# Kernel tuning notes

Measured on AMD Instinct MI355X. Metric: run time of the kernel, lower is better.

The kernel has to match this reference:

```python
import jax, jax.numpy as jnp
import numpy as np

LN_EPS = 1e-5  # torch LayerNorm default
MODES = 4


def setup_inputs() -> dict:
    key = jax.random.key(0)
    ks = jax.random.split(key, 5)
    B, S, H = 4, 4096, 1024
    nh, dk = 16, H // 16
    scale = 1.0 / (H * H)
    # frequency mode selection: random shuffle of range(S//2), take 4, sorted (seeded for determinism)
    rng = np.random.default_rng(0)
    index = jnp.asarray(np.sort(rng.permutation(S // 2)[:MODES]).astype(np.int32))
    return {
        "x": jax.random.normal(ks[0], (B, S, H), dtype=jnp.float32),
        "Wq": jax.random.normal(ks[1], (H, H), dtype=jnp.float32) * np.sqrt(2.0 / (H + dk)),
        "bq": jnp.zeros((H,), dtype=jnp.float32),
        "wr": scale * jax.random.uniform(ks[2], (nh, dk, dk, MODES), dtype=jnp.float32),
        "wi": scale * jax.random.uniform(ks[3], (nh, dk, dk, MODES), dtype=jnp.float32),
        "gamma": jnp.ones((H,), dtype=jnp.float32),
        "beta": jnp.zeros((H,), dtype=jnp.float32),
        "index": index,
    }


def reference(x, Wq, bq, wr, wi, gamma, beta, index):
    B, S, H = x.shape
    nh, dk = wr.shape[0], wr.shape[1]
    # q projection and head split: (B,S,H) -> (B,S,nh,dk) -> (B,nh,dk,S)
    q = (x @ Wq.T + bq).reshape(B, S, nh, dk).transpose(0, 2, 3, 1)
    x_ft = jnp.fft.rfft(q, axis=-1)                 # (B,nh,dk,S//2+1) complex
    xm = x_ft[..., index]                           # gather selected modes: (B,nh,dk,M)
    w = wr + 1j * wi                                # (nh,dk,dk,M) complex
    ym = jnp.einsum('bhim,hiom->bhom', xm, w)       # per-mode complex matmul
    # faithful: results written at slots 0..M-1 of out_ft (loop writes out_ft[...,wi])
    out_ft = jnp.zeros((B, nh, dk, S // 2 + 1), dtype=ym.dtype).at[..., :ym.shape[-1]].set(ym)
    x_if = jnp.fft.irfft(out_ft, n=S, axis=-1)      # (B,nh,dk,S) real
    # faithful permute(0,3,2,1).view: flattens as dk-major over heads
    out = x_if.transpose(0, 3, 2, 1).reshape(B, S, H)
    # dropout is identity in eval mode
    y = out + x
    mu = jnp.mean(y, axis=-1, keepdims=True)
    var = jnp.var(y, axis=-1, keepdims=True)
    return (y - mu) * jax.lax.rsqrt(var + LN_EPS) * gamma + beta
```

## Files before the change

kernel.cpp:

```cpp
#include <hip/hip_runtime.h>
#include <math.h>

#define BB 4
#define SS 4096
#define HH 1024
#define NH 16
#define DK 64
#define NMODES 4
#define NSB 128
#define SCHUNK (SS/NSB)
#define PPLANE ((size_t)BB * NSB * HH)
#define TWO_PI 6.28318530717958647692f

__global__ __launch_bounds__(256) void kA_dft(const float* __restrict__ x,
                                              const int* __restrict__ index,
                                              float* __restrict__ P) {
    __shared__ float tab[SCHUNK * 8];
    int t  = threadIdx.x;
    int sb = blockIdx.x & (NSB - 1);
    int b  = blockIdx.x >> 7;

    if (t < SCHUNK * NMODES) {
        int sl = t >> 2, m = t & 3;
        int k  = index[m];
        int sv = sb * SCHUNK + sl;
        int r  = (k * sv) & (SS - 1);
        float ang = (float)r * (TWO_PI / (float)SS);
        float sn, cs;
        sincosf(ang, &sn, &cs);
        tab[sl * 8 + m * 2]     = cs;
        tab[sl * 8 + m * 2 + 1] = sn;
    }
    __syncthreads();

    int c0 = t * 4;
    float acc[4][8];
    #pragma unroll
    for (int e = 0; e < 4; ++e)
        #pragma unroll
        for (int q = 0; q < 8; ++q) acc[e][q] = 0.f;

    const float* xp = x + ((size_t)(b * SS + sb * SCHUNK)) * HH + c0;
    #pragma unroll 4
    for (int r = 0; r < SCHUNK; ++r) {
        float4 xv = *(const float4*)(xp + (size_t)r * HH);
        float4 t0 = *(const float4*)&tab[r * 8];
        float4 t1 = *(const float4*)&tab[r * 8 + 4];
        float xe;
        #pragma unroll
        for (int e = 0; e < 4; ++e) {
            xe = (e == 0) ? xv.x : (e == 1) ? xv.y : (e == 2) ? xv.z : xv.w;
            acc[e][0] += xe * t0.x;  acc[e][1] -= xe * t0.y;
            acc[e][2] += xe * t0.z;  acc[e][3] -= xe * t0.w;
            acc[e][4] += xe * t1.x;  acc[e][5] -= xe * t1.y;
            acc[e][6] += xe * t1.z;  acc[e][7] -= xe * t1.w;
        }
    }
    size_t base = (size_t)(b * NSB + sb) * HH + c0;
    #pragma unroll
    for (int q = 0; q < 8; ++q) {
        *(float4*)&P[q * PPLANE + base] =
            make_float4(acc[0][q], acc[1][q], acc[2][q], acc[3][q]);
    }
}

__global__ __launch_bounds__(256) void kA2_reduce(const float* __restrict__ P,
                                                  float* __restrict__ G) {
    int g = blockIdx.x * 256 + threadIdx.x;
    int j = g & (HH - 1);
    int q = (g >> 10) & 7;
    int b = g >> 13;
    const float* pp = P + q * PPLANE + (size_t)b * NSB * HH + j;
    float s = 0.f;
    #pragma unroll 16
    for (int sb = 0; sb < NSB; ++sb)
        s += pp[(size_t)sb * HH];
    G[g] = s;
}

__global__ __launch_bounds__(256) void kB_proj(const float* __restrict__ Wq,
                                               const float* __restrict__ bq,
                                               const int* __restrict__ index,
                                               const float* __restrict__ G,
                                               float* __restrict__ XM) {
    __shared__ float Gs[8 * HH];
    int t  = threadIdx.x;
    int cb = blockIdx.x & 63;
    int b  = blockIdx.x >> 6;
    {
        const float4* gsrc = (const float4*)(G + (size_t)b * 8 * HH);
        float4* gdst = (float4*)Gs;
        for (int u = t; u < 2 * HH; u += 256) gdst[u] = gsrc[u];
    }
    __syncthreads();

    int cl = t >> 4, jq = t & 15;
    int c = cb * 16 + cl;
    float acc[8] = {0.f,0.f,0.f,0.f,0.f,0.f,0.f,0.f};
    for (int j0 = jq * 4; j0 < HH; j0 += 64) {
        float4 wv = *(const float4*)&Wq[(size_t)c * HH + j0];
        #pragma unroll
        for (int q = 0; q < 8; ++q) {
            float4 gv = *(const float4*)&Gs[q * HH + j0];
            acc[q] += wv.x * gv.x + wv.y * gv.y + wv.z * gv.z + wv.w * gv.w;
        }
    }
    #pragma unroll
    for (int q = 0; q < 8; ++q) {
        acc[q] += __shfl_xor(acc[q], 1);
        acc[q] += __shfl_xor(acc[q], 2);
        acc[q] += __shfl_xor(acc[q], 4);
        acc[q] += __shfl_xor(acc[q], 8);
    }
    if (jq == 0) {
        float bias = bq[c];
        #pragma unroll
        for (int m = 0; m < NMODES; ++m)
            if (index[m] == 0) acc[2 * m] += bias * (float)SS;
        float* o = XM + ((size_t)(b * HH + c)) * 8;
        *(float4*)o       = make_float4(acc[0], acc[1], acc[2], acc[3]);
        *(float4*)(o + 4) = make_float4(acc[4], acc[5], acc[6], acc[7]);
    }
}

#define KC_IQ 8
#define KC_II (DK / KC_IQ)
__global__ __launch_bounds__(512) void kC_modes(const float* __restrict__ wr,
                                                const float* __restrict__ wi,
                                                const float* __restrict__ XM,
                                                float* __restrict__ CF) {
    __shared__ float xs[DK * 8];
    __shared__ float red[KC_IQ][DK][9];
    int t = threadIdx.x;
    int o = t & 63, iq = t >> 6;
    int h = blockIdx.x & 15;
    int b = blockIdx.x >> 4;
    for (int u = t; u < DK * 8; u += 512)
        xs[u] = XM[((size_t)(b * HH + h * DK)) * 8 + u];
    __syncthreads();

    float re[4] = {0.f,0.f,0.f,0.f}, im[4] = {0.f,0.f,0.f,0.f};
    #pragma unroll
    for (int ii = 0; ii < KC_II; ++ii) {
        int i = iq * KC_II + ii;
        float4 wrv = *(const float4*)&wr[(((size_t)(h * DK + i)) * DK + o) * 4];
        float4 wiv = *(const float4*)&wi[(((size_t)(h * DK + i)) * DK + o) * 4];
        float xr, xi;
        xr = xs[i * 8 + 0]; xi = xs[i * 8 + 1];
        re[0] += xr * wrv.x - xi * wiv.x;  im[0] += xr * wiv.x + xi * wrv.x;
        xr = xs[i * 8 + 2]; xi = xs[i * 8 + 3];
        re[1] += xr * wrv.y - xi * wiv.y;  im[1] += xr * wiv.y + xi * wrv.y;
        xr = xs[i * 8 + 4]; xi = xs[i * 8 + 5];
        re[2] += xr * wrv.z - xi * wiv.z;  im[2] += xr * wiv.z + xi * wrv.z;
        xr = xs[i * 8 + 6]; xi = xs[i * 8 + 7];
        re[3] += xr * wrv.w - xi * wiv.w;  im[3] += xr * wiv.w + xi * wrv.w;
    }
    #pragma unroll
    for (int m = 0; m < 4; ++m) {
        red[iq][o][2 * m]     = re[m];
        red[iq][o][2 * m + 1] = im[m];
    }
    __syncthreads();
    if (iq == 0) {
        float rr[8];
        #pragma unroll
        for (int q = 0; q < 8; ++q) {
            float s = 0.f;
            #pragma unroll
            for (int g = 0; g < KC_IQ; ++g) s += red[g][o][q];
            rr[q] = s;
        }
        int co = o * NH + h;
        const float inv = 1.0f / (float)SS;
        float* cp = CF + ((size_t)(b * HH + co)) * 8;
        cp[0] =  rr[0] * inv;
        cp[1] =  2.0f * rr[2] * inv;
        cp[2] = -2.0f * rr[3] * inv;
        cp[3] =  2.0f * rr[4] * inv;
        cp[4] = -2.0f * rr[5] * inv;
        cp[5] =  2.0f * rr[6] * inv;
        cp[6] = -2.0f * rr[7] * inv;
        cp[7] =  0.0f;
    }
}

#define KD_ROWS 16
#define KD_RB 8
__global__ __launch_bounds__(256) void kD_out(const float* __restrict__ x,
                                              const float* __restrict__ CF,
                                              const float* __restrict__ gamma,
                                              const float* __restrict__ beta,
                                              float* __restrict__ out) {
    __shared__ float trig[KD_ROWS][2];
    __shared__ float red[4][KD_RB][2];
    int t  = threadIdx.x;
    int b  = blockIdx.x >> 8;
    int s0 = (blockIdx.x & 255) * KD_ROWS;
    int c0 = t * 4;

    if (t < KD_ROWS) {
        float ang = (float)(s0 + t) * (TWO_PI / (float)SS);
        float sn, cs;
        sincosf(ang, &sn, &cs);
        trig[t][0] = cs;
        trig[t][1] = sn;
    }

    const float* cp = CF + (size_t)b * HH * 8 + (size_t)c0 * 8;
    float4 cfa[8];
    #pragma unroll
    for (int e = 0; e < 4; ++e) {
        cfa[2 * e]     = *(const float4*)(cp + e * 8);
        cfa[2 * e + 1] = *(const float4*)(cp + e * 8 + 4);
    }
    float4 g4 = *(const float4*)&gamma[c0];
    float4 b4 = *(const float4*)&beta[c0];
    int w = t >> 6, lane = t & 63;
    __syncthreads();

    for (int batch = 0; batch < KD_ROWS / KD_RB; ++batch) {
        float4 yv[KD_RB];
        #pragma unroll
        for (int r = 0; r < KD_RB; ++r) {
            int s = s0 + batch * KD_RB + r;
            yv[r] = *(const float4*)&x[((size_t)(b * SS + s)) * HH + c0];
        }
        float sm[KD_RB], sq[KD_RB];
        #pragma unroll
        for (int r = 0; r < KD_RB; ++r) {
            int ri = batch * KD_RB + r;
            float c1 = trig[ri][0], s1 = trig[ri][1];
            float c2 = c1 * c1 - s1 * s1, s2 = 2.f * s1 * c1;
            float c3 = c2 * c1 - s2 * s1, s3 = s2 * c1 + c2 * s1;
            float ye[4];
            #pragma unroll
            for (int e = 0; e < 4; ++e) {
                float xe = (e == 0) ? yv[r].x : (e == 1) ? yv[r].y
                         : (e == 2) ? yv[r].z : yv[r].w;
                float4 A = cfa[2 * e], Bv = cfa[2 * e + 1];
                ye[e] = xe + A.x + A.y * c1 + A.z * s1 + A.w * c2
                           + Bv.x * s2 + Bv.y * c3 + Bv.z * s3;
            }
            yv[r] = make_float4(ye[0], ye[1], ye[2], ye[3]);
            sm[r] = ye[0] + ye[1] + ye[2] + ye[3];
            sq[r] = ye[0]*ye[0] + ye[1]*ye[1] + ye[2]*ye[2] + ye[3]*ye[3];
        }
        #pragma unroll
        for (int off = 1; off < 64; off <<= 1) {
            #pragma unroll
            for (int r = 0; r < KD_RB; ++r) {
                sm[r] += __shfl_xor(sm[r], off);
                sq[r] += __shfl_xor(sq[r], off);
            }
        }
        if (lane == 0) {
            #pragma unroll
            for (int r = 0; r < KD_RB; ++r) {
                red[w][r][0] = sm[r];
                red[w][r][1] = sq[r];
            }
        }
        __syncthreads();
        #pragma unroll
        for (int r = 0; r < KD_RB; ++r) {
            int s = s0 + batch * KD_RB + r;
            float tot  = red[0][r][0] + red[1][r][0] + red[2][r][0] + red[3][r][0];
            float totq = red[0][r][1] + red[1][r][1] + red[2][r][1] + red[3][r][1];
            float mean = tot * (1.0f / (float)HH);
            float var  = totq * (1.0f / (float)HH) - mean * mean;
            float rs = rsqrtf(var + 1e-5f);
            float4 o4;
            o4.x = (yv[r].x - mean) * rs * g4.x + b4.x;
            o4.y = (yv[r].y - mean) * rs * g4.y + b4.y;
            o4.z = (yv[r].z - mean) * rs * g4.z + b4.z;
            o4.w = (yv[r].w - mean) * rs * g4.w + b4.w;
            *(float4*)&out[((size_t)(b * SS + s)) * HH + c0] = o4;
        }
        __syncthreads();
    }
}

extern "C" void kernel_launch(void* const* d_in, const int* in_sizes, int n_in,
                              void* d_out, int out_size, void* d_ws, size_t ws_size,
                              hipStream_t stream) {
    const float* x     = (const float*)d_in[0];
    const float* Wq    = (const float*)d_in[1];
    const float* bq    = (const float*)d_in[2];
    const float* wr    = (const float*)d_in[3];
    const float* wi    = (const float*)d_in[4];
    const float* gamma = (const float*)d_in[5];
    const float* beta  = (const float*)d_in[6];
    const int*   index = (const int*)d_in[7];
    float* out = (float*)d_out;
    float* ws  = (float*)d_ws;

    const size_t nP     = PPLANE * 8;
    const size_t nSmall = (size_t)BB * HH * 8;

    float *P, *G, *XM, *CF;
    if (ws_size >= (nP + 3 * nSmall) * sizeof(float)) {
        P  = ws;
        G  = P + nP;
        XM = G + nSmall;
        CF = XM + nSmall;
    } else {
        P  = out;
        G  = ws;
        XM = G + nSmall;
        CF = XM + nSmall;
    }

    hipLaunchKernelGGL(kA_dft,     dim3(BB * NSB), dim3(256), 0, stream, x, index, P);
    hipLaunchKernelGGL(kA2_reduce, dim3(BB * HH * 8 / 256), dim3(256), 0, stream, P, G);
    hipLaunchKernelGGL(kB_proj,    dim3(BB * 64), dim3(256), 0, stream, Wq, bq, index, G, XM);
    hipLaunchKernelGGL(kC_modes,   dim3(BB * NH), dim3(512), 0, stream, wr, wi, XM, CF);
    hipLaunchKernelGGL(kD_out,     dim3(BB * (SS / KD_ROWS)), dim3(256), 0, stream, x, CF, gamma, beta, out);
}
```

Before: 61.73 us.

## Fuse reduce, projection and mode kernels into one cooperative kernel with grid syncs

Merges the partial-sum reduction, the Wq projection and the per-mode complex matmul into a single cooperative kernel of 256 blocks, separated by grid-wide syncs. This replaces three launches and removes the inter-kernel gaps. The reduction now splits each sum across two threads, and the mode stage runs with 256 threads per block instead of 512. The DFT loop unroll also goes from 4 to 8. The cost is that grid.sync barriers add their own latency, and the mode stage keeps only 64 of the 256 blocks busy.

```diff
diff --git a/kernel.cpp b/kernel.cpp
--- a/kernel.cpp
+++ b/kernel.cpp
@@ -1,5 +1,8 @@
 #include <hip/hip_runtime.h>
+#include <hip/hip_cooperative_groups.h>
 #include <math.h>
+
+namespace cg = cooperative_groups;
 
 #define BB 4
 #define SS 4096
@@ -41,7 +44,7 @@
         for (int q = 0; q < 8; ++q) acc[e][q] = 0.f;
 
     const float* xp = x + ((size_t)(b * SS + sb * SCHUNK)) * HH + c0;
-    #pragma unroll 4
+    #pragma unroll 8
     for (int r = 0; r < SCHUNK; ++r) {
         float4 xv = *(const float4*)(xp + (size_t)r * HH);
         float4 t0 = *(const float4*)&tab[r * 8];
@@ -64,123 +67,130 @@
     }
 }
 
-__global__ __launch_bounds__(256) void kA2_reduce(const float* __restrict__ P,
-                                                  float* __restrict__ G) {
-    int g = blockIdx.x * 256 + threadIdx.x;
-    int j = g & (HH - 1);
-    int q = (g >> 10) & 7;
-    int b = g >> 13;
-    const float* pp = P + q * PPLANE + (size_t)b * NSB * HH + j;
-    float s = 0.f;
-    #pragma unroll 16
-    for (int sb = 0; sb < NSB; ++sb)
-        s += pp[(size_t)sb * HH];
-    G[g] = s;
-}
-
-__global__ __launch_bounds__(256) void kB_proj(const float* __restrict__ Wq,
-                                               const float* __restrict__ bq,
-                                               const int* __restrict__ index,
-                                               const float* __restrict__ G,
-                                               float* __restrict__ XM) {
-    __shared__ float Gs[8 * HH];
-    int t  = threadIdx.x;
-    int cb = blockIdx.x & 63;
-    int b  = blockIdx.x >> 6;
+__global__ __launch_bounds__(256) void kMid(const float* __restrict__ P,
+                                            const float* __restrict__ Wq,
+                                            const float* __restrict__ bq,
+                                            const int* __restrict__ index,
+                                            const float* __restrict__ wr,
+                                            const float* __restrict__ wi,
+                                            float* __restrict__ G,
+                                            float* __restrict__ XM,
+                                            float* __restrict__ CF) {
+    cg::grid_group grid = cg::this_grid();
+    __shared__ float lds[10240];
+    int t = threadIdx.x, bid = blockIdx.x;
+
     {
+        int i = bid * 256 + t;
+        int g = i >> 1;
+        int half = i & 1;
+        int j = g & (HH - 1);
+        int q = (g >> 10) & 7;
+        int b = g >> 13;
+        const float* pp = P + q * PPLANE + (size_t)b * NSB * HH
+                        + (size_t)(half * (NSB / 2)) * HH + j;
+        float s = 0.f;
+        #pragma unroll 16
+        for (int sb = 0; sb < NSB / 2; ++sb)
+            s += pp[(size_t)sb * HH];
+        float other = __shfl_xor(s, 1);
+        if (half == 0) G[g] = s + other;
+    }
+    __threadfence();
+    grid.sync();
+
+    {
+        int cb = bid & 63;
+        int b  = bid >> 6;
         const float4* gsrc = (const float4*)(G + (size_t)b * 8 * HH);
-        float4* gdst = (float4*)Gs;
+        float4* gdst = (float4*)lds;
         for (int u = t; u < 2 * HH; u += 256) gdst[u] = gsrc[u];
-    }
-    __syncthreads();
-
-    int cl = t >> 4, jq = t & 15;
-    int c = cb * 16 + cl;
-    float acc[8] = {0.f,0.f,0.f,0.f,0.f,0.f,0.f,0.f};
-    for (int j0 = jq * 4; j0 < HH; j0 += 64) {
-        float4 wv = *(const float4*)&Wq[(size_t)c * HH + j0];
+        __syncthreads();
+
+        int cl = t >> 4, jq = t & 15;
+        int c = cb * 16 + cl;
+        float acc[8] = {0.f,0.f,0.f,0.f,0.f,0.f,0.f,0.f};
+        for (int j0 = jq * 4; j0 < HH; j0 += 64) {
+            float4 wv = *(const float4*)&Wq[(size_t)c * HH + j0];
+            #pragma unroll
+            for (int q = 0; q < 8; ++q) {
+                float4 gv = *(const float4*)&lds[q * HH + j0];
+                acc[q] += wv.x * gv.x + wv.y * gv.y + wv.z * gv.z + wv.w * gv.w;
+            }
+        }
         #pragma unroll
         for (int q = 0; q < 8; ++q) {
-            float4 gv = *(const float4*)&Gs[q * HH + j0];
-            acc[q] += wv.x * gv.x + wv.y * gv.y + wv.z * gv.z + wv.w * gv.w;
-        }
-    }
-    #pragma unroll
-    for (int q = 0; q < 8; ++q) {
-        acc[q] += __shfl_xor(acc[q], 1);
-        acc[q] += __shfl_xor(acc[q], 2);
-        acc[q] += __shfl_xor(acc[q], 4);
-        acc[q] += __shfl_xor(acc[q], 8);
-    }
-    if (jq == 0) {
-        float bias = bq[c];
-        #pragma unroll
-        for (int m = 0; m < NMODES; ++m)
-            if (index[m] == 0) acc[2 * m] += bias * (float)SS;
-        float* o = XM + ((size_t)(b * HH + c)) * 8;
-        *(float4*)o       = make_float4(acc[0], acc[1], acc[2], acc[3]);
-        *(float4*)(o + 4) = make_float4(acc[4], acc[5], acc[6], acc[7]);
-    }
-}
-
-#define KC_IQ 8
-#define KC_II (DK / KC_IQ)
-__global__ __launch_bounds__(512) void kC_modes(const float* __restrict__ wr,
-                                                const float* __restrict__ wi,
-                                                const float* __restrict__ XM,
-                                                float* __restrict__ CF) {
-    __shared__ float xs[DK * 8];
-    __shared__ float red[KC_IQ][DK][9];
-    int t = threadIdx.x;
-    int o = t & 63, iq = t >> 6;
-    int h = blockIdx.x & 15;
-    int b = blockIdx.x >> 4;
-    for (int u = t; u < DK * 8; u += 512)
-        xs[u] = XM[((size_t)(b * HH + h * DK)) * 8 + u];
-    __syncthreads();
-
-    float re[4] = {0.f,0.f,0.f,0.f}, im[4] = {0.f,0.f,0.f,0.f};
-    #pragma unroll
-    for (int ii = 0; ii < KC_II; ++ii) {
-        int i = iq * KC_II + ii;
-        float4 wrv = *(const float4*)&wr[(((size_t)(h * DK + i)) * DK + o) * 4];
-        float4 wiv = *(const float4*)&wi[(((size_t)(h * DK + i)) * DK + o) * 4];
-        float xr, xi;
-        xr = xs[i * 8 + 0]; xi = xs[i * 8 + 1];
-        re[0] += xr * wrv.x - xi * wiv.x;  im[0] += xr * wiv.x + xi * wrv.x;
-        xr = xs[i * 8 + 2]; xi = xs[i * 8 + 3];
-        re[1] += xr * wrv.y - xi * wiv.y;  im[1] += xr * wiv.y + xi * wrv.y;
-        xr = xs[i * 8 + 4]; xi = xs[i * 8 + 5];
-        re[2] += xr * wrv.z - xi * wiv.z;  im[2] += xr * wiv.z + xi * wrv.z;
-        xr = xs[i * 8 + 6]; xi = xs[i * 8 + 7];
-        re[3] += xr * wrv.w - xi * wiv.w;  im[3] += xr * wiv.w + xi * wrv.w;
-    }
-    #pragma unroll
-    for (int m = 0; m < 4; ++m) {
-        red[iq][o][2 * m]     = re[m];
-        red[iq][o][2 * m + 1] = im[m];
-    }
-    __syncthreads();
-    if (iq == 0) {
-        float rr[8];
-        #pragma unroll
-        for (int q = 0; q < 8; ++q) {
-            float s = 0.f;
-            #pragma unroll
-            for (int g = 0; g < KC_IQ; ++g) s += red[g][o][q];
-            rr[q] = s;
-        }
-        int co = o * NH + h;
-        const float inv = 1.0f / (float)SS;
-        float* cp = CF + ((size_t)(b * HH + co)) * 8;
-        cp[0] =  rr[0] * inv;
-        cp[1] =  2.0f * rr[2] * inv;
-        cp[2] = -2.0f * rr[3] * inv;
-        cp[3] =  2.0f * rr[4] * inv;
-        cp[4] = -2.0f * rr[5] * inv;
-        cp[5] =  2.0f * rr[6] * inv;
-        cp[6] = -2.0f * rr[7] * inv;
-        cp[7] =  0.0f;
+            acc[q] += __shfl_xor(acc[q], 1);
+            acc[q] += __shfl_xor(acc[q], 2);
+            acc[q] += __shfl_xor(acc[q], 4);
+            acc[q] += __shfl_xor(acc[q], 8);
+        }
+        if (jq == 0) {
+            float bias = bq[c];
+            #pragma unroll
+            for (int m = 0; m < NMODES; ++m)
+                if (index[m] == 0) acc[2 * m] += bias * (float)SS;
+            float* o = XM + ((size_t)(b * HH + c)) * 8;
+            *(float4*)o       = make_float4(acc[0], acc[1], acc[2], acc[3]);
+            *(float4*)(o + 4) = make_float4(acc[4], acc[5], acc[6], acc[7]);
+        }
+    }
+    __threadfence();
+    grid.sync();
+
+    if (bid < BB * NH) {
+        float* xs = lds;
+        float (*red)[DK][9] = (float(*)[DK][9])(lds + DK * 8);
+        int o = t & 63, iq = t >> 6;
+        int h = bid & 15;
+        int b = bid >> 4;
+        for (int u = t; u < DK * 8; u += 256)
+            xs[u] = XM[((size_t)(b * HH + h * DK)) * 8 + u];
+        __syncthreads();
+
+        float re[4] = {0.f,0.f,0.f,0.f}, im[4] = {0.f,0.f,0.f,0.f};
+        #pragma unroll
+        for (int ii = 0; ii < 16; ++ii) {
+            int i = iq * 16 + ii;
+            float4 wrv = *(const float4*)&wr[(((size_t)(h * DK + i)) * DK + o) * 4];
+            float4 wiv = *(const float4*)&wi[(((size_t)(h * DK + i)) * DK + o) * 4];
+            float xr, xi;
+            xr = xs[i * 8 + 0]; xi = xs[i * 8 + 1];
+            re[0] += xr * wrv.x - xi * wiv.x;  im[0] += xr * wiv.x + xi * wrv.x;
+            xr = xs[i * 8 + 2]; xi = xs[i * 8 + 3];
+            re[1] += xr * wrv.y - xi * wiv.y;  im[1] += xr * wiv.y + xi * wrv.y;
+            xr = xs[i * 8 + 4]; xi = xs[i * 8 + 5];
+            re[2] += xr * wrv.z - xi * wiv.z;  im[2] += xr * wiv.z + xi * wrv.z;
+            xr = xs[i * 8 + 6]; xi = xs[i * 8 + 7];
+            re[3] += xr * wrv.w - xi * wiv.w;  im[3] += xr * wiv.w + xi * wrv.w;
+        }
+        #pragma unroll
+        for (int m = 0; m < 4; ++m) {
+            red[iq][o][2 * m]     = re[m];
+            red[iq][o][2 * m + 1] = im[m];
+        }
+        __syncthreads();
+        if (iq == 0) {
+            float rr[8];
+            #pragma unroll
+            for (int q = 0; q < 8; ++q) {
+                float s = 0.f;
+                #pragma unroll
+                for (int g2 = 0; g2 < 4; ++g2) s += red[g2][o][q];
+                rr[q] = s;
+            }
+            int co = o * NH + h;
+            const float inv = 1.0f / (float)SS;
+            float* cp = CF + ((size_t)(b * HH + co)) * 8;
+            cp[0] =  rr[0] * inv;
+            cp[1] =  2.0f * rr[2] * inv;
+            cp[2] = -2.0f * rr[3] * inv;
+            cp[3] =  2.0f * rr[4] * inv;
+            cp[4] = -2.0f * rr[5] * inv;
+            cp[5] =  2.0f * rr[6] * inv;
+            cp[6] =  2.0f * -rr[7] * inv;
+            cp[7] =  0.0f;
+        }
     }
 }
 
@@ -310,9 +320,15 @@
         CF = XM + nSmall;
     }
 
-    hipLaunchKernelGGL(kA_dft,     dim3(BB * NSB), dim3(256), 0, stream, x, index, P);
-    hipLaunchKernelGGL(kA2_reduce, dim3(BB * HH * 8 / 256), dim3(256), 0, stream, P, G);
-    hipLaunchKernelGGL(kB_proj,    dim3(BB * 64), dim3(256), 0, stream, Wq, bq, index, G, XM);
-    hipLaunchKernelGGL(kC_modes,   dim3(BB * NH), dim3(512), 0, stream, wr, wi, XM, CF);
-    hipLaunchKernelGGL(kD_out,     dim3(BB * (SS / KD_ROWS)), dim3(256), 0, stream, x, CF, gamma, beta, out);
+    hipLaunchKernelGGL(kA_dft, dim3(BB * NSB), dim3(256), 0, stream, x, index, P);
+
+    {
+        void* args[] = {(void*)&P, (void*)&Wq, (void*)&bq, (void*)&index,
+                        (void*)&wr, (void*)&wi, (void*)&G, (void*)&XM, (void*)&CF};
+        hipLaunchCooperativeKernel((const void*)kMid, dim3(256), dim3(256),
+                                   args, 0, stream);
+    }
+
+    hipLaunchKernelGGL(kD_out, dim3(BB * (SS / KD_ROWS)), dim3(256), 0, stream,
+                       x, CF, gamma, beta, out);
 }
```

New measurement: 152.9 us. 148% more time.
